# Kernel optimization log

Hardware: AMD Instinct MI355X
Metric: run time of the kernel (lower is better)

The kernel has to match this reference:

```python
import jax, jax.numpy as jnp
import numpy as np

B, C, L = 4, 256, 4096
C8 = C // 8

def setup_inputs() -> dict:
    key = jax.random.key(0)
    ks = jax.random.split(key, 8)
    s = 1.0 / np.sqrt(C)
    x = jax.random.normal(ks[0], (B, C, L), dtype=jnp.float32)
    Wq = jax.random.normal(ks[1], (C8, C), dtype=jnp.float32) * s
    bq = jax.random.normal(ks[2], (C8,), dtype=jnp.float32) * s
    Wk = jax.random.normal(ks[3], (C8, C), dtype=jnp.float32) * s
    bk = jax.random.normal(ks[4], (C8,), dtype=jnp.float32) * s
    Wv = jax.random.normal(ks[5], (C, C), dtype=jnp.float32) * s
    bv = jax.random.normal(ks[6], (C,), dtype=jnp.float32) * s
    gamma = jax.random.normal(ks[7], (1,), dtype=jnp.float32) * 0.1
    return {"x": x, "Wq": Wq, "bq": bq, "Wk": Wk, "bk": bk, "Wv": Wv, "bv": bv, "gamma": gamma}

def reference(x, Wq, bq, Wk, bk, Wv, bv, gamma):
    # pointwise conv1d == channel matmul: [O,C] x [B,C,L] -> [B,O,L]
    q = jnp.einsum('oc,bcl->bol', Wq, x) + bq[None, :, None]   # [B, C8, L]
    k = jnp.einsum('oc,bcl->bol', Wk, x) + bk[None, :, None]   # [B, C8, L]
    v = jnp.einsum('oc,bcl->bol', Wv, x) + bv[None, :, None]   # [B, C,  L]
    # attention[b,i,j] = sum_c q[b,c,i] * k[b,c,j]
    attn = jnp.einsum('bci,bcj->bij', q, k)                    # [B, L, L]
    attn = jax.nn.softmax(attn, axis=-1)
    # out[b,c,i] = sum_j v[b,c,j] * attn[b,i,j]
    out = jnp.einsum('bcj,bij->bci', v, attn)                  # [B, C, L]
    return gamma * out + x
```

## Files before the change

kernel.cpp:

```cpp
#include <hip/hip_runtime.h>
#include <math.h>

#define BB 4
#define CC 256
#define LL 4096
#define DD 32
#define LOG2E 1.44269504088896f

typedef __attribute__((ext_vector_type(8))) short short8;
typedef __attribute__((ext_vector_type(4))) short short4v;
typedef __attribute__((ext_vector_type(4))) float f32x4;
typedef __attribute__((ext_vector_type(16))) float f32x16;
typedef __attribute__((ext_vector_type(4))) unsigned int uint4v;
typedef __attribute__((ext_vector_type(2))) unsigned int uint2v;

#define BARRIER() asm volatile("s_waitcnt lgkmcnt(0)\n\ts_barrier" ::: "memory")

__device__ inline float fast_exp2(float x) {
#if __has_builtin(__builtin_amdgcn_exp2f)
  return __builtin_amdgcn_exp2f(x);
#else
  return exp2f(x);
#endif
}

#define PACK8_STORE(EX0,EX1,EX2,EX3,EX4,EX5,EX6,EX7, DSTPTR)                         \
  {                                                                                  \
    unsigned pw0, pw1, pw2, pw3;                                                     \
    asm("v_cvt_pk_bf16_f32 %0, %1, %2" : "=v"(pw0) : "v"(EX0), "v"(EX1));            \
    asm("v_cvt_pk_bf16_f32 %0, %1, %2" : "=v"(pw1) : "v"(EX2), "v"(EX3));            \
    asm("v_cvt_pk_bf16_f32 %0, %1, %2" : "=v"(pw2) : "v"(EX4), "v"(EX5));            \
    asm("v_cvt_pk_bf16_f32 %0, %1, %2" : "=v"(pw3) : "v"(EX6), "v"(EX7));            \
    asm("v_permlane32_swap_b32 %0, %1" : "+v"(pw0), "+v"(pw2));                      \
    asm("v_permlane32_swap_b32 %0, %1" : "+v"(pw1), "+v"(pw3));                      \
    uint4v pu; pu.x = pw0; pu.y = pw1; pu.z = pw2; pu.w = pw3;                       \
    *(uint4v*)(DSTPTR) = pu;                                                         \
  }

__global__ __launch_bounds__(256) void wprep_kernel(
    const float* __restrict__ Wq, const float* __restrict__ Wk, const float* __restrict__ Wv,
    unsigned short* __restrict__ wf)
{
  const int t = threadIdx.x;
  const int g = blockIdx.x * 4 + (t >> 6);
  const int lane = t & 63, ql = lane & 31, hi = lane >> 5;
  const int tile = g >> 4, chunk = g & 15;
  const int cin = chunk * 16 + hi * 8;
  const float* src;
  float sc = 1.0f;
  if (tile == 0)      { src = Wq + (size_t)ql * CC; sc = LOG2E; }
  else if (tile == 1) { src = Wk + (size_t)ql * CC; }
  else                { src = Wv + (size_t)(32 * (tile - 2) + ql) * CC; }
  const f32x4 a = *(const f32x4*)(src + cin);
  const f32x4 b2 = *(const f32x4*)(src + cin + 4);
  unsigned w0, w1, w2, w3;
  const float f0 = a[0] * sc, f1 = a[1] * sc, f2 = a[2] * sc, f3 = a[3] * sc;
  const float f4 = b2[0] * sc, f5 = b2[1] * sc, f6 = b2[2] * sc, f7 = b2[3] * sc;
  asm("v_cvt_pk_bf16_f32 %0, %1, %2" : "=v"(w0) : "v"(f0), "v"(f1));
  asm("v_cvt_pk_bf16_f32 %0, %1, %2" : "=v"(w1) : "v"(f2), "v"(f3));
  asm("v_cvt_pk_bf16_f32 %0, %1, %2" : "=v"(w2) : "v"(f4), "v"(f5));
  asm("v_cvt_pk_bf16_f32 %0, %1, %2" : "=v"(w3) : "v"(f6), "v"(f7));
  uint4v u; u.x = w0; u.y = w1; u.z = w2; u.w = w3;
  *(uint4v*)(wf + ((size_t)g * 64 + lane) * 8) = u;
}

__global__ __launch_bounds__(512, 4) void qkv_kernel(
    const float* __restrict__ x, const unsigned short* __restrict__ wf,
    const float* __restrict__ bq, const float* __restrict__ bk, const float* __restrict__ bv,
    unsigned short* __restrict__ qF, unsigned short* __restrict__ kF,
    unsigned short* __restrict__ vF)
{
  __shared__ __align__(16) unsigned short xb[16 * 64 * 8];

  const int t = threadIdx.x;
  const int w = t >> 6, lane = t & 63, ql = lane & 31, hi = lane >> 5;
  const int blk = blockIdx.x;
  const int b  = (blk & 7) >> 1;
  const int it = ((blk >> 3) << 1) + (blk & 1);
  const int i0 = it * 32;

  #pragma unroll
  for (int e = 0; e < 2; ++e) {
    const int cc = 2 * w + e;
    const float* xs = x + ((size_t)(b * CC + cc * 16 + hi * 8)) * LL + i0 + ql;
    float f[8];
    #pragma unroll
    for (int j = 0; j < 8; ++j) f[j] = xs[(size_t)j * LL];
    unsigned w0, w1, w2, w3;
    asm("v_cvt_pk_bf16_f32 %0, %1, %2" : "=v"(w0) : "v"(f[0]), "v"(f[1]));
    asm("v_cvt_pk_bf16_f32 %0, %1, %2" : "=v"(w1) : "v"(f[2]), "v"(f[3]));
    asm("v_cvt_pk_bf16_f32 %0, %1, %2" : "=v"(w2) : "v"(f[4]), "v"(f[5]));
    asm("v_cvt_pk_bf16_f32 %0, %1, %2" : "=v"(w3) : "v"(f[6]), "v"(f[7]));
    uint4v u; u.x = w0; u.y = w1; u.z = w2; u.w = w3;
    *(uint4v*)&xb[(cc * 64 + lane) * 8] = u;
  }
  __syncthreads();

  const f32x16 z16 = {0.f,0.f,0.f,0.f,0.f,0.f,0.f,0.f,0.f,0.f,0.f,0.f,0.f,0.f,0.f,0.f};

  {
    f32x16 D = z16;
    #pragma unroll
    for (int c = 0; c < 16; ++c) {
      const short8 xc = *(const short8*)&xb[(c * 64 + lane) * 8];
      const short8 wv = *(const short8*)(wf + ((size_t)((2 + w) * 16 + c) * 64 + lane) * 8);
      D = __builtin_amdgcn_mfma_f32_32x32x16_bf16(xc, wv, D, 0, 0, 0);
    }
    const float bvv = bv[32 * w + ql];
    #pragma unroll
    for (int r = 0; r < 16; ++r) D[r] += bvv;
    #pragma unroll
    for (int s = 0; s < 2; ++s) {
      unsigned short* dst = vF + (((size_t)(b * 256 + 2 * it + s) * 8 + w) * 64 + lane) * 8;
      PACK8_STORE(D[8*s+0], D[8*s+1], D[8*s+2], D[8*s+3],
                  D[8*s+4], D[8*s+5], D[8*s+6], D[8*s+7], dst);
    }
  }

  if (w < 2) {
    const float* bsrc = w ? bk : bq;
    const float bscale = w ? 1.0f : LOG2E;
    float br[16];
    #pragma unroll
    for (int r = 0; r < 16; ++r)
      br[r] = bsrc[(r & 3) + 8 * (r >> 2) + 4 * hi] * bscale;
    f32x16 D = z16;
    #pragma unroll
    for (int c = 0; c < 16; ++c) {
      const short8 xc = *(const short8*)&xb[(c * 64 + lane) * 8];
      const short8 wa = *(const short8*)(wf + ((size_t)(w * 16 + c) * 64 + lane) * 8);
      D = __builtin_amdgcn_mfma_f32_32x32x16_bf16(wa, xc, D, 0, 0, 0);
    }
    #pragma unroll
    for (int r = 0; r < 16; ++r) D[r] += br[r];
    unsigned short* basef = w ? kF : qF;
    #pragma unroll
    for (int s = 0; s < 2; ++s) {
      unsigned short* dst = basef + (((size_t)(b * 128 + it) * 2 + s) * 64 + lane) * 8;
      PACK8_STORE(D[8*s+0], D[8*s+1], D[8*s+2], D[8*s+3],
                  D[8*s+4], D[8*s+5], D[8*s+6], D[8*s+7], dst);
    }
  }
}

__global__ __launch_bounds__(768, 3) void attn_kernel(
    const unsigned short* __restrict__ qF, const unsigned short* __restrict__ kF,
    const unsigned short* __restrict__ vF, const float* __restrict__ x,
    const float* __restrict__ gamma_p, float* __restrict__ out)
{
  __shared__ __align__(16) unsigned short P[2 * 8 * 2 * 2 * 512];
  __shared__ float l_lds[8][2][64];

  const int t = threadIdx.x;
  const int w = t >> 6, lane = t & 63, ql = lane & 31, hi = lane >> 5;
  const int blk = blockIdx.x;
  const int b  = (blk & 7) >> 1;
  const int it = ((blk >> 3) << 1) + (blk & 1);
  const int i0 = it * 64;

  if (w < 8) {
    const int pw = w;
    short8 qB[2][2];
    #pragma unroll
    for (int qt = 0; qt < 2; ++qt)
      #pragma unroll
      for (int c = 0; c < 2; ++c)
        qB[qt][c] = *(const short8*)(qF +
            (((size_t)(b * 128 + it * 2 + qt) * 2 + c) * 64 + lane) * 8);
    short8 kA[2];
    #pragma unroll
    for (int c = 0; c < 2; ++c)
      kA[c] = *(const short8*)(kF + (((size_t)(b * 128 + pw) * 2 + c) * 64 + lane) * 8);
    float l_r[2] = {0.f, 0.f};
    const f32x16 z16 = {0.f,0.f,0.f,0.f,0.f,0.f,0.f,0.f,0.f,0.f,0.f,0.f,0.f,0.f,0.f,0.f};

    auto produce = [&](int ss, int buf) {
      f32x16 S[2];
      __builtin_amdgcn_s_setprio(1);
      #pragma unroll
      for (int qt = 0; qt < 2; ++qt)
        S[qt] = __builtin_amdgcn_mfma_f32_32x32x16_bf16(kA[0], qB[qt][0], z16, 0, 0, 0);
      #pragma unroll
      for (int qt = 0; qt < 2; ++qt)
        S[qt] = __builtin_amdgcn_mfma_f32_32x32x16_bf16(kA[1], qB[qt][1], S[qt], 0, 0, 0);
      __builtin_amdgcn_s_setprio(0);
      const int ntile = ((ss + 1) & 15) * 8 + pw;
      #pragma unroll
      for (int c = 0; c < 2; ++c)
        kA[c] = *(const short8*)(kF + (((size_t)(b * 128 + ntile) * 2 + c) * 64 + lane) * 8);
      #pragma unroll
      for (int qt = 0; qt < 2; ++qt) {
        float ex[16];
        #pragma unroll
        for (int r = 0; r < 16; ++r) ex[r] = fast_exp2(S[qt][r]);
        l_r[qt] += ((((ex[0] + ex[1]) + (ex[2] + ex[3])) + ((ex[4] + ex[5]) + (ex[6] + ex[7])))
                 + (((ex[8] + ex[9]) + (ex[10] + ex[11])) + ((ex[12] + ex[13]) + (ex[14] + ex[15]))));
        #pragma unroll
        for (int c = 0; c < 2; ++c) {
          unsigned short* dst = &P[(((buf * 8 + pw) * 2 + qt) * 2 + c) * 512 + hi * 256 + ql * 8];
          PACK8_STORE(ex[8*c+0], ex[8*c+1], ex[8*c+2], ex[8*c+3],
                      ex[8*c+4], ex[8*c+5], ex[8*c+6], ex[8*c+7], dst);
        }
      }
    };

    produce(0, 0);
    __syncthreads();
    for (int i = 0; i < 16; ++i) {
      if (i < 15) produce(i + 1, (i + 1) & 1);
      BARRIER();
    }
    l_lds[pw][0][lane] = l_r[0];
    l_lds[pw][1][lane] = l_r[1];
    BARRIER();
  } else {
    const int mq = w - 8;
    const unsigned short* vroot = vF + (size_t)b * (256 * 8 * 512) + lane * 8;
    f32x16 O[2][2];
    #pragma unroll
    for (int mi = 0; mi < 2; ++mi)
      #pragma unroll
      for (int qt = 0; qt < 2; ++qt) {
        const f32x16 z16 = {0.f,0.f,0.f,0.f,0.f,0.f,0.f,0.f,0.f,0.f,0.f,0.f,0.f,0.f,0.f,0.f};
        O[mi][qt] = z16;
      }
    short8 vA[4][2];
    #pragma unroll
    for (int s = 0; s < 4; ++s)
      #pragma unroll
      for (int mi = 0; mi < 2; ++mi)
        vA[s][mi] = *(const short8*)(vroot + ((size_t)(s * 8 + 2 * mq + mi)) * 512);
    __syncthreads();

    short8 pb[3][2];
    for (int i = 0; i < 16; ++i) {
      const int buf = i & 1;
      #pragma unroll
      for (int s = 0; s < 2; ++s)
        #pragma unroll
        for (int qt = 0; qt < 2; ++qt)
          pb[s][qt] = *(const short8*)(&P[((((buf * 8 + 0) * 2 + qt) * 2 + s) * 512)
                                          + hi * 256 + ql * 8]);
      #pragma unroll
      for (int s = 0; s < 16; ++s) {
        if (s < 14) {
          const int ns = s + 2, kk = ns >> 1, c = ns & 1;
          #pragma unroll
          for (int qt = 0; qt < 2; ++qt)
            pb[ns % 3][qt] = *(const short8*)(&P[((((buf * 8 + kk) * 2 + qt) * 2 + c) * 512)
                                                 + hi * 256 + ql * 8]);
        }
        __builtin_amdgcn_s_setprio(1);
        #pragma unroll
        for (int mi = 0; mi < 2; ++mi)
          #pragma unroll
          for (int qt = 0; qt < 2; ++qt)
            O[mi][qt] = __builtin_amdgcn_mfma_f32_32x32x16_bf16(vA[s & 3][mi], pb[s % 3][qt],
                                                                O[mi][qt], 0, 0, 0);
        __builtin_amdgcn_s_setprio(0);
        const int kg = (i * 16 + s + 4) & 255;
        #pragma unroll
        for (int mi = 0; mi < 2; ++mi)
          vA[s & 3][mi] = *(const short8*)(vroot + ((size_t)(kg * 8 + 2 * mq + mi)) * 512);
      }
      BARRIER();
    }
    BARRIER();

    const float gam = gamma_p[0];
    float inv_l[2];
    #pragma unroll
    for (int qt = 0; qt < 2; ++qt) {
      float s = 0.f;
      #pragma unroll
      for (int pw = 0; pw < 8; ++pw)
        s += l_lds[pw][qt][ql] + l_lds[pw][qt][ql + 32];
      inv_l[qt] = 1.0f / s;
    }
    #pragma unroll
    for (int mi = 0; mi < 2; ++mi)
      #pragma unroll
      for (int qt = 0; qt < 2; ++qt)
        #pragma unroll
        for (int r = 0; r < 16; ++r) {
          const int ch = 64 * mq + 32 * mi + (r & 3) + 8 * (r >> 2) + 4 * hi;
          const int ii = i0 + 32 * qt + ql;
          const size_t idx = ((size_t)b * CC + ch) * LL + ii;
          out[idx] = gam * O[mi][qt][r] * inv_l[qt] + x[idx];
        }
  }
}

extern "C" void kernel_launch(void* const* d_in, const int* in_sizes, int n_in,
                              void* d_out, int out_size, void* d_ws, size_t ws_size,
                              hipStream_t stream) {
  const float* x     = (const float*)d_in[0];
  const float* Wq    = (const float*)d_in[1];
  const float* bq    = (const float*)d_in[2];
  const float* Wk    = (const float*)d_in[3];
  const float* bk    = (const float*)d_in[4];
  const float* Wv    = (const float*)d_in[5];
  const float* bv    = (const float*)d_in[6];
  const float* gamma = (const float*)d_in[7];
  float* out = (float*)d_out;

  unsigned short* qF = (unsigned short*)d_ws;
  unsigned short* kF = qF + (size_t)BB * LL * DD;
  unsigned short* vF = kF + (size_t)BB * LL * DD;
  unsigned short* wf = (unsigned short*)d_out;

  wprep_kernel<<<40, 256, 0, stream>>>(Wq, Wk, Wv, wf);
  qkv_kernel<<<512, 512, 0, stream>>>(x, wf, bq, bk, bv, qF, kF, vF);
  attn_kernel<<<256, 768, 0, stream>>>(qF, kF, vF, x, gamma, out);
}
```

Measured before the change: 129.8 us.

## Rebalance attention warps: 4 softmax producers, 8 PV consumers split over key halves

The attention kernel changes its warp split from 8 producer warps (QK^T plus exp) and 4 PV consumer warps to 4 producers that each handle two key tiles and 8 consumers. The consumers split the key dimension into two halves, and their partial outputs are reduced through an LDS buffer that is unioned with the P buffer. The aim is to shift work toward the PV matrix multiply, which has more MFMA work per step, and so balance the pipeline. The cost is a doubled per-warp exp load on the producers, an extra reduction through shared memory, and extra barriers at the end.

```diff
diff --git a/kernel.cpp b/kernel.cpp
--- a/kernel.cpp
+++ b/kernel.cpp
@@ -8,11 +8,9 @@
 #define LOG2E 1.44269504088896f
 
 typedef __attribute__((ext_vector_type(8))) short short8;
-typedef __attribute__((ext_vector_type(4))) short short4v;
 typedef __attribute__((ext_vector_type(4))) float f32x4;
 typedef __attribute__((ext_vector_type(16))) float f32x16;
 typedef __attribute__((ext_vector_type(4))) unsigned int uint4v;
-typedef __attribute__((ext_vector_type(2))) unsigned int uint2v;
 
 #define BARRIER() asm volatile("s_waitcnt lgkmcnt(0)\n\ts_barrier" ::: "memory")
 
@@ -53,9 +51,9 @@
   else                { src = Wv + (size_t)(32 * (tile - 2) + ql) * CC; }
   const f32x4 a = *(const f32x4*)(src + cin);
   const f32x4 b2 = *(const f32x4*)(src + cin + 4);
-  unsigned w0, w1, w2, w3;
   const float f0 = a[0] * sc, f1 = a[1] * sc, f2 = a[2] * sc, f3 = a[3] * sc;
   const float f4 = b2[0] * sc, f5 = b2[1] * sc, f6 = b2[2] * sc, f7 = b2[3] * sc;
+  unsigned w0, w1, w2, w3;
   asm("v_cvt_pk_bf16_f32 %0, %1, %2" : "=v"(w0) : "v"(f0), "v"(f1));
   asm("v_cvt_pk_bf16_f32 %0, %1, %2" : "=v"(w1) : "v"(f2), "v"(f3));
   asm("v_cvt_pk_bf16_f32 %0, %1, %2" : "=v"(w2) : "v"(f4), "v"(f5));
@@ -148,8 +146,11 @@
     const unsigned short* __restrict__ vF, const float* __restrict__ x,
     const float* __restrict__ gamma_p, float* __restrict__ out)
 {
-  __shared__ __align__(16) unsigned short P[2 * 8 * 2 * 2 * 512];
-  __shared__ float l_lds[8][2][64];
+  __shared__ union __align__(16) {
+    unsigned short P[2 * 8 * 2 * 2 * 512];
+    float Om[4][4][64][16];
+  } sm;
+  __shared__ float l_lds[4][2][64];
 
   const int t = threadIdx.x;
   const int w = t >> 6, lane = t & 63, ql = lane & 31, hi = lane >> 5;
@@ -157,8 +158,9 @@
   const int b  = (blk & 7) >> 1;
   const int it = ((blk >> 3) << 1) + (blk & 1);
   const int i0 = it * 64;
-
-  if (w < 8) {
+  const f32x16 z16 = {0.f,0.f,0.f,0.f,0.f,0.f,0.f,0.f,0.f,0.f,0.f,0.f,0.f,0.f,0.f,0.f};
+
+  if (w < 4) {
     const int pw = w;
     short8 qB[2][2];
     #pragma unroll
@@ -167,39 +169,47 @@
       for (int c = 0; c < 2; ++c)
         qB[qt][c] = *(const short8*)(qF +
             (((size_t)(b * 128 + it * 2 + qt) * 2 + c) * 64 + lane) * 8);
-    short8 kA[2];
-    #pragma unroll
-    for (int c = 0; c < 2; ++c)
-      kA[c] = *(const short8*)(kF + (((size_t)(b * 128 + pw) * 2 + c) * 64 + lane) * 8);
+    short8 kA[2][2];
+    #pragma unroll
+    for (int e = 0; e < 2; ++e)
+      #pragma unroll
+      for (int c = 0; c < 2; ++c)
+        kA[e][c] = *(const short8*)(kF +
+            (((size_t)(b * 128 + 2 * pw + e) * 2 + c) * 64 + lane) * 8);
     float l_r[2] = {0.f, 0.f};
-    const f32x16 z16 = {0.f,0.f,0.f,0.f,0.f,0.f,0.f,0.f,0.f,0.f,0.f,0.f,0.f,0.f,0.f,0.f};
 
     auto produce = [&](int ss, int buf) {
-      f32x16 S[2];
-      __builtin_amdgcn_s_setprio(1);
-      #pragma unroll
-      for (int qt = 0; qt < 2; ++qt)
-        S[qt] = __builtin_amdgcn_mfma_f32_32x32x16_bf16(kA[0], qB[qt][0], z16, 0, 0, 0);
-      #pragma unroll
-      for (int qt = 0; qt < 2; ++qt)
-        S[qt] = __builtin_amdgcn_mfma_f32_32x32x16_bf16(kA[1], qB[qt][1], S[qt], 0, 0, 0);
-      __builtin_amdgcn_s_setprio(0);
-      const int ntile = ((ss + 1) & 15) * 8 + pw;
-      #pragma unroll
-      for (int c = 0; c < 2; ++c)
-        kA[c] = *(const short8*)(kF + (((size_t)(b * 128 + ntile) * 2 + c) * 64 + lane) * 8);
-      #pragma unroll
-      for (int qt = 0; qt < 2; ++qt) {
-        float ex[16];
-        #pragma unroll
-        for (int r = 0; r < 16; ++r) ex[r] = fast_exp2(S[qt][r]);
-        l_r[qt] += ((((ex[0] + ex[1]) + (ex[2] + ex[3])) + ((ex[4] + ex[5]) + (ex[6] + ex[7])))
-                 + (((ex[8] + ex[9]) + (ex[10] + ex[11])) + ((ex[12] + ex[13]) + (ex[14] + ex[15]))));
-        #pragma unroll
-        for (int c = 0; c < 2; ++c) {
-          unsigned short* dst = &P[(((buf * 8 + pw) * 2 + qt) * 2 + c) * 512 + hi * 256 + ql * 8];
-          PACK8_STORE(ex[8*c+0], ex[8*c+1], ex[8*c+2], ex[8*c+3],
-                      ex[8*c+4], ex[8*c+5], ex[8*c+6], ex[8*c+7], dst);
+      #pragma unroll
+      for (int e = 0; e < 2; ++e) {
+        const int kk = 2 * pw + e;
+        f32x16 S[2];
+        __builtin_amdgcn_s_setprio(1);
+        #pragma unroll
+        for (int qt = 0; qt < 2; ++qt)
+          S[qt] = __builtin_amdgcn_mfma_f32_32x32x16_bf16(kA[e][0], qB[qt][0], z16, 0, 0, 0);
+        #pragma unroll
+        for (int qt = 0; qt < 2; ++qt)
+          S[qt] = __builtin_amdgcn_mfma_f32_32x32x16_bf16(kA[e][1], qB[qt][1], S[qt], 0, 0, 0);
+        __builtin_amdgcn_s_setprio(0);
+        const int ntile = ((ss + 1) & 15) * 8 + kk;
+        #pragma unroll
+        for (int c = 0; c < 2; ++c)
+          kA[e][c] = *(const short8*)(kF +
+              (((size_t)(b * 128 + ntile) * 2 + c) * 64 + lane) * 8);
+        #pragma unroll
+        for (int qt = 0; qt < 2; ++qt) {
+          float ex[16];
+          #pragma unroll
+          for (int r = 0; r < 16; ++r) ex[r] = fast_exp2(S[qt][r]);
+          l_r[qt] += ((((ex[0] + ex[1]) + (ex[2] + ex[3])) + ((ex[4] + ex[5]) + (ex[6] + ex[7])))
+                   + (((ex[8] + ex[9]) + (ex[10] + ex[11])) + ((ex[12] + ex[13]) + (ex[14] + ex[15]))));
+          #pragma unroll
+          for (int c = 0; c < 2; ++c) {
+            unsigned short* dst =
+                &sm.P[(((buf * 8 + kk) * 2 + qt) * 2 + c) * 512 + hi * 256 + ql * 8];
+            PACK8_STORE(ex[8*c+0], ex[8*c+1], ex[8*c+2], ex[8*c+3],
+                        ex[8*c+4], ex[8*c+5], ex[8*c+6], ex[8*c+7], dst);
+          }
         }
       }
     };
@@ -213,42 +223,44 @@
     l_lds[pw][0][lane] = l_r[0];
     l_lds[pw][1][lane] = l_r[1];
     BARRIER();
+    BARRIER();
   } else {
-    const int mq = w - 8;
+    const int cw = w - 4, kh = cw >> 2, mq = cw & 3;
     const unsigned short* vroot = vF + (size_t)b * (256 * 8 * 512) + lane * 8;
     f32x16 O[2][2];
     #pragma unroll
     for (int mi = 0; mi < 2; ++mi)
       #pragma unroll
-      for (int qt = 0; qt < 2; ++qt) {
-        const f32x16 z16 = {0.f,0.f,0.f,0.f,0.f,0.f,0.f,0.f,0.f,0.f,0.f,0.f,0.f,0.f,0.f,0.f};
-        O[mi][qt] = z16;
-      }
+      for (int qt = 0; qt < 2; ++qt) O[mi][qt] = z16;
     short8 vA[4][2];
     #pragma unroll
-    for (int s = 0; s < 4; ++s)
+    for (int s = 0; s < 4; ++s) {
+      const int kg = 8 * kh + s;
       #pragma unroll
       for (int mi = 0; mi < 2; ++mi)
-        vA[s][mi] = *(const short8*)(vroot + ((size_t)(s * 8 + 2 * mq + mi)) * 512);
+        vA[s][mi] = *(const short8*)(vroot + ((size_t)(kg * 8 + 2 * mq + mi)) * 512);
+    }
     __syncthreads();
 
     short8 pb[3][2];
     for (int i = 0; i < 16; ++i) {
       const int buf = i & 1;
       #pragma unroll
-      for (int s = 0; s < 2; ++s)
+      for (int s = 0; s < 2; ++s) {
+        const int kk = 4 * kh + (s >> 1), c = s & 1;
         #pragma unroll
         for (int qt = 0; qt < 2; ++qt)
-          pb[s][qt] = *(const short8*)(&P[((((buf * 8 + 0) * 2 + qt) * 2 + s) * 512)
-                                          + hi * 256 + ql * 8]);
-      #pragma unroll
-      for (int s = 0; s < 16; ++s) {
-        if (s < 14) {
-          const int ns = s + 2, kk = ns >> 1, c = ns & 1;
+          pb[s][qt] = *(const short8*)(&sm.P[((((buf * 8 + kk) * 2 + qt) * 2 + c) * 512)
+                                             + hi * 256 + ql * 8]);
+      }
+      #pragma unroll
+      for (int s = 0; s < 8; ++s) {
+        if (s < 6) {
+          const int ns = s + 2, kk = 4 * kh + (ns >> 1), c = ns & 1;
           #pragma unroll
           for (int qt = 0; qt < 2; ++qt)
-            pb[ns % 3][qt] = *(const short8*)(&P[((((buf * 8 + kk) * 2 + qt) * 2 + c) * 512)
-                                                 + hi * 256 + ql * 8]);
+            pb[ns % 3][qt] = *(const short8*)(&sm.P[((((buf * 8 + kk) * 2 + qt) * 2 + c) * 512)
+                                                    + hi * 256 + ql * 8]);
         }
         __builtin_amdgcn_s_setprio(1);
         #pragma unroll
@@ -258,7 +270,8 @@
             O[mi][qt] = __builtin_amdgcn_mfma_f32_32x32x16_bf16(vA[s & 3][mi], pb[s % 3][qt],
                                                                 O[mi][qt], 0, 0, 0);
         __builtin_amdgcn_s_setprio(0);
-        const int kg = (i * 16 + s + 4) & 255;
+        const int ls = s + 4;
+        const int kg = ((i + (ls >> 3)) & 15) * 16 + 8 * kh + (ls & 7);
         #pragma unroll
         for (int mi = 0; mi < 2; ++mi)
           vA[s & 3][mi] = *(const short8*)(vroot + ((size_t)(kg * 8 + 2 * mq + mi)) * 512);
@@ -266,28 +279,39 @@
       BARRIER();
     }
     BARRIER();
-
-    const float gam = gamma_p[0];
-    float inv_l[2];
-    #pragma unroll
-    for (int qt = 0; qt < 2; ++qt) {
-      float s = 0.f;
-      #pragma unroll
-      for (int pw = 0; pw < 8; ++pw)
-        s += l_lds[pw][qt][ql] + l_lds[pw][qt][ql + 32];
-      inv_l[qt] = 1.0f / s;
-    }
-    #pragma unroll
-    for (int mi = 0; mi < 2; ++mi)
-      #pragma unroll
-      for (int qt = 0; qt < 2; ++qt)
-        #pragma unroll
-        for (int r = 0; r < 16; ++r) {
-          const int ch = 64 * mq + 32 * mi + (r & 3) + 8 * (r >> 2) + 4 * hi;
-          const int ii = i0 + 32 * qt + ql;
-          const size_t idx = ((size_t)b * CC + ch) * LL + ii;
-          out[idx] = gam * O[mi][qt][r] * inv_l[qt] + x[idx];
+    if (kh == 1) {
+      #pragma unroll
+      for (int mi = 0; mi < 2; ++mi)
+        #pragma unroll
+        for (int qt = 0; qt < 2; ++qt)
+          *(f32x16*)&sm.Om[mq][mi * 2 + qt][lane][0] = O[mi][qt];
+    }
+    BARRIER();
+    if (kh == 0) {
+      const float gam = gamma_p[0];
+      float inv_l[2];
+      #pragma unroll
+      for (int qt = 0; qt < 2; ++qt) {
+        float s = 0.f;
+        #pragma unroll
+        for (int pw = 0; pw < 4; ++pw)
+          s += l_lds[pw][qt][ql] + l_lds[pw][qt][ql + 32];
+        inv_l[qt] = 1.0f / s;
+      }
+      #pragma unroll
+      for (int mi = 0; mi < 2; ++mi)
+        #pragma unroll
+        for (int qt = 0; qt < 2; ++qt) {
+          const f32x16 om = *(const f32x16*)&sm.Om[mq][mi * 2 + qt][lane][0];
+          #pragma unroll
+          for (int r = 0; r < 16; ++r) {
+            const int ch = 64 * mq + 32 * mi + (r & 3) + 8 * (r >> 2) + 4 * hi;
+            const int ii = i0 + 32 * qt + ql;
+            const size_t idx = ((size_t)b * CC + ch) * LL + ii;
+            out[idx] = gam * (O[mi][qt][r] + om[r]) * inv_l[qt] + x[idx];
+          }
         }
+    }
   }
 }
 
```

Result: no change. 132.1 us (+1.7%).
